# Kernel optimization log

Hardware: AMD Instinct MI355X
Metric: run time of the kernel (lower is better)

The kernel has to match this reference:

```python
import jax, jax.numpy as jnp
import numpy as np

N, E, H, R = 20000, 400000, 128, 20


def setup_inputs() -> dict:
    key = jax.random.key(0)
    ks = jax.random.split(key, 12)
    inv_h = 1.0 / np.sqrt(H)
    inv_r = 1.0 / np.sqrt(R)
    return {
        "s": jax.random.normal(ks[0], (N, H), jnp.float32),
        "v": jax.random.normal(ks[1], (N, 3, H), jnp.float32),
        "edge_rbf": jax.random.normal(ks[2], (E, R), jnp.float32),
        "edge_cutoff": jax.random.uniform(ks[3], (E,), jnp.float32),
        "edge_vec": jax.random.normal(ks[4], (E, 3), jnp.float32),
        "W1": jax.random.normal(ks[5], (H, H), jnp.float32) * inv_h,
        "b1": jnp.zeros((H,), jnp.float32),
        "W2": jax.random.normal(ks[6], (H, 3 * H), jnp.float32) * inv_h,
        "b2": jnp.zeros((3 * H,), jnp.float32),
        "Wr": jax.random.normal(ks[7], (R, 3 * H), jnp.float32) * inv_r,
        "br": jnp.zeros((3 * H,), jnp.float32),
        "edge_index": jax.random.randint(ks[8], (2, E), 0, N, jnp.int64),
    }


def reference(s, v, edge_rbf, edge_cutoff, edge_vec, W1, b1, W2, b2, Wr, br, edge_index):
    i, j = edge_index[0], edge_index[1]
    n = s.shape[0]
    # rbf projection modulated by cutoff: [E, 3H]
    W = (edge_rbf @ Wr + br) * edge_cutoff[:, None]
    # scalar MLP on gathered source features: [E, 3H]
    h = jax.nn.silu(s[j] @ W1 + b1)
    x = (h @ W2 + b2) * W
    x_ss, x_sv, x_vv = jnp.split(x, 3, axis=-1)  # each [E, H]
    ds = jax.ops.segment_sum(x_ss, i, num_segments=n)
    # dv1: outer product of edge direction with gated scalars -> [E,3,H]
    dv1 = jax.ops.segment_sum(x_sv[:, None, :] * edge_vec[:, :, None], i, num_segments=n)
    # equivariant term: project v_j onto edge direction, re-expand
    inner = jnp.sum(v[j] * edge_vec[:, :, None], axis=1)  # [E, H]
    dv2 = jax.ops.segment_sum((inner * x_vv)[:, None, :] * edge_vec[:, :, None], i, num_segments=n)
    return ds, dv1 + dv2
```

## Files before the change

### kernel.cpp

```cpp
#include <hip/hip_runtime.h>
#include <hip/hip_bf16.h>

#define HDIM 128
#define H3   384
#define RDIM 20
#define NPB  16
#define EPB  128

typedef unsigned short u16;
typedef unsigned int   u32;
typedef __attribute__((ext_vector_type(8))) short short8v;
typedef __attribute__((ext_vector_type(4))) float f32x4;

__device__ __forceinline__ u16 f2bf(float f) {
    __hip_bfloat16 h = __float2bfloat16(f);
    return *(u16*)&h;
}
__device__ __forceinline__ float bf2f(u16 u) {
    union { u32 i; float f; } x; x.i = (u32)u << 16; return x.f;
}
__device__ __forceinline__ float bflo(u32 u) {
    union { u32 i; float f; } x; x.i = u << 16; return x.f;
}
__device__ __forceinline__ float bfhi(u32 u) {
    union { u32 i; float f; } x; x.i = u & 0xffff0000u; return x.f;
}
__device__ __forceinline__ u32 pk(float lo, float hi) {
    return (u32)f2bf(lo) | ((u32)f2bf(hi) << 16);
}

__global__ __launch_bounds__(128) void node_mlp_kernel(
    const float* __restrict__ s, const float* __restrict__ W1,
    const float* __restrict__ b1, const float* __restrict__ W2,
    const float* __restrict__ b2, const float* __restrict__ v,
    u32* __restrict__ P3, int N)
{
    __shared__ float sS[NPB][HDIM];
    __shared__ float sH[NPB][HDIM];
    const int t  = threadIdx.x;
    const int n0 = blockIdx.x * NPB;

    #pragma unroll
    for (int n = 0; n < NPB; ++n) {
        int node = n0 + n;
        sS[n][t] = (node < N) ? s[(size_t)node * HDIM + t] : 0.f;
    }
    __syncthreads();

    float acc[NPB];
    #pragma unroll
    for (int n = 0; n < NPB; ++n) acc[n] = 0.f;
    for (int k = 0; k < HDIM; ++k) {
        float w = W1[k * HDIM + t];
        #pragma unroll
        for (int n = 0; n < NPB; ++n) acc[n] += sS[n][k] * w;
    }
    float bb = b1[t];
    #pragma unroll
    for (int n = 0; n < NPB; ++n) {
        float z = acc[n] + bb;
        sH[n][t] = z / (1.f + __expf(-z));
    }
    __syncthreads();

    float a0[NPB], a1[NPB], a2[NPB];
    #pragma unroll
    for (int n = 0; n < NPB; ++n) { a0[n] = 0.f; a1[n] = 0.f; a2[n] = 0.f; }
    for (int k2 = 0; k2 < HDIM / 2; ++k2) {
        float2 hv[NPB];
        #pragma unroll
        for (int n = 0; n < NPB; ++n) hv[n] = ((const float2*)sH[n])[k2];
        #pragma unroll
        for (int kk = 0; kk < 2; ++kk) {
            int k = 2 * k2 + kk;
            float w0 = W2[k * H3 + t];
            float w1 = W2[k * H3 + t + 128];
            float w2 = W2[k * H3 + t + 256];
            #pragma unroll
            for (int n = 0; n < NPB; ++n) {
                float h = kk ? hv[n].y : hv[n].x;
                a0[n] += h * w0;
                a1[n] += h * w1;
                a2[n] += h * w2;
            }
        }
    }
    float c0 = b2[t], c1 = b2[t + 128], c2 = b2[t + 256];
    #pragma unroll
    for (int n = 0; n < NPB; ++n) {
        int node = n0 + n;
        if (node < N) {
            size_t vb = (size_t)node * H3;
            float vx = v[vb + t], vy = v[vb + 128 + t], vz = v[vb + 256 + t];
            size_t pb = (size_t)node * H3 + t;
            P3[pb]       = pk(a0[n] + c0, a1[n] + c1);
            P3[pb + 128] = pk(a2[n] + c2, vx);
            P3[pb + 256] = pk(vy, vz);
        }
    }
}

__global__ void hist_kernel(const int* __restrict__ eidx, int* __restrict__ counts, int E)
{
    int e = blockIdx.x * 256 + threadIdx.x;
    if (e < E) atomicAdd(&counts[eidx[e]], 1);
}

__global__ __launch_bounds__(1024) void scan_kernel(
    const int* __restrict__ counts, int* __restrict__ rstart,
    int* __restrict__ cursor, int N)
{
    __shared__ int part[1024];
    const int t = threadIdx.x;
    const int C = 20;
    int loc[C];
    int s = 0;
    #pragma unroll
    for (int q = 0; q < C; ++q) {
        int idx = t * C + q;
        int c = (idx < N) ? counts[idx] : 0;
        loc[q] = s; s += c;
    }
    part[t] = s;
    __syncthreads();
    for (int off = 1; off < 1024; off <<= 1) {
        int vv = (t >= off) ? part[t - off] : 0;
        __syncthreads();
        part[t] += vv;
        __syncthreads();
    }
    int boff = (t > 0) ? part[t - 1] : 0;
    #pragma unroll
    for (int q = 0; q < C; ++q) {
        int idx = t * C + q;
        if (idx < N) {
            int st = boff + loc[q];
            rstart[idx] = st;
            cursor[idx] = st;
        }
    }
    if (t == 1023) rstart[N] = part[1023];
}

__global__ void scatter_kernel(const int* __restrict__ eidx, int* __restrict__ cursor,
                               int* __restrict__ eord, int E)
{
    int e = blockIdx.x * 256 + threadIdx.x;
    if (e < E) {
        int i = eidx[e];
        int pos = atomicAdd(&cursor[i], 1);
        eord[pos] = e;
    }
}

__global__ __launch_bounds__(256) void wgemm_kernel(
    const int* __restrict__ eord, const float* __restrict__ rbf,
    const float* __restrict__ cutoff, const float* __restrict__ Wr,
    const float* __restrict__ br, u16* __restrict__ Ws, int E)
{
    const int lane    = threadIdx.x & 63;
    const int wave    = threadIdx.x >> 6;
    const int g       = lane >> 4;
    const int m       = lane & 15;
    const int colhalf = wave & 1;
    const int wgrp    = wave >> 1;

    short8v bfrag[12];
    float   brt[12];
    #pragma unroll
    for (int n = 0; n < 12; ++n) {
        int col = colhalf * 192 + n * 16 + m;
        short8v f;
        #pragma unroll
        for (int j = 0; j < 8; ++j) {
            int k = 8 * g + j;
            f[j] = (k < RDIM) ? (short)f2bf(Wr[k * H3 + col]) : (short)0;
        }
        bfrag[n] = f;
        brt[n] = br[col];
    }

    const int PBI = 256;
    for (int it = 0; it < PBI / 32; ++it) {
        int pbase = blockIdx.x * PBI + it * 32 + wgrp * 16;
        if (pbase >= E) break;

        short8v af;
        int posA = pbase + m;
        if (posA < E && g < 3) {
            const float* rr = rbf + (size_t)eord[posA] * RDIM;
            if (g < 2) {
                float4 r0 = *(const float4*)(rr + 8 * g);
                float4 r1 = *(const float4*)(rr + 8 * g + 4);
                af[0] = (short)f2bf(r0.x); af[1] = (short)f2bf(r0.y);
                af[2] = (short)f2bf(r0.z); af[3] = (short)f2bf(r0.w);
                af[4] = (short)f2bf(r1.x); af[5] = (short)f2bf(r1.y);
                af[6] = (short)f2bf(r1.z); af[7] = (short)f2bf(r1.w);
            } else {
                float4 r0 = *(const float4*)(rr + 16);
                af[0] = (short)f2bf(r0.x); af[1] = (short)f2bf(r0.y);
                af[2] = (short)f2bf(r0.z); af[3] = (short)f2bf(r0.w);
                af[4] = 0; af[5] = 0; af[6] = 0; af[7] = 0;
            }
        } else {
            #pragma unroll
            for (int j = 0; j < 8; ++j) af[j] = 0;
        }

        float cut[4];
        #pragma unroll
        for (int r = 0; r < 4; ++r) {
            int pos = pbase + 4 * g + r;
            cut[r] = (pos < E) ? cutoff[eord[pos]] : 0.f;
        }

        #pragma unroll
        for (int n = 0; n < 12; ++n) {
            f32x4 c = {0.f, 0.f, 0.f, 0.f};
            c = __builtin_amdgcn_mfma_f32_16x16x32_bf16(af, bfrag[n], c, 0, 0, 0);
            int col = colhalf * 192 + n * 16 + m;
            #pragma unroll
            for (int r = 0; r < 4; ++r) {
                int pos = pbase + 4 * g + r;
                if (pos < E)
                    Ws[(size_t)pos * H3 + col] = f2bf((c[r] + brt[n]) * cut[r]);
            }
        }
    }
}

__global__ __launch_bounds__(128) void edge_kernel(
    const int* __restrict__ eord, const int* __restrict__ eidx,
    const float* __restrict__ evec, const u16* __restrict__ Ws,
    const u32* __restrict__ P3, float* __restrict__ ds,
    float* __restrict__ dv, int E)
{
    const int t    = threadIdx.x;
    const int base = blockIdx.x * EPB;
    const int cnt  = min(EPB, E - base);

    __shared__ int   sI[EPB], sJ[EPB];
    __shared__ float sVx[EPB], sVy[EPB], sVz[EPB];

    if (t < cnt) {
        int e  = eord[base + t];
        sI[t]  = eidx[e];
        sJ[t]  = eidx[E + e] * H3;
        sVx[t] = evec[3 * e];
        sVy[t] = evec[3 * e + 1];
        sVz[t] = evec[3 * e + 2];
    }
    __syncthreads();

    const u16* wp = Ws + (size_t)base * H3 + t;

    int   cur  = sI[0];
    float accs = 0.f, accx = 0.f, accy = 0.f, accz = 0.f;

    u32 ca, cb, cc; u16 w0c, w1c, w2c;
    {
        int idx = sJ[0] + t;
        ca = P3[idx]; cb = P3[idx + 128]; cc = P3[idx + 256];
        w0c = wp[0]; w1c = wp[128]; w2c = wp[256];
    }

    for (int q = 0; q < cnt; ++q) {
        u32 na = 0, nb = 0, nc = 0; u16 w0n = 0, w1n = 0, w2n = 0;
        if (q + 1 < cnt) {
            int idx = sJ[q + 1] + t;
            na = P3[idx]; nb = P3[idx + 128]; nc = P3[idx + 256];
            const u16* wq = wp + (size_t)(q + 1) * H3;
            w0n = wq[0]; w1n = wq[128]; w2n = wq[256];
        }
        if (sI[q] != cur) {
            atomicAdd(&ds[(size_t)cur * HDIM + t], accs);
            size_t dvi = (size_t)cur * H3;
            atomicAdd(&dv[dvi + t],       accx);
            atomicAdd(&dv[dvi + 128 + t], accy);
            atomicAdd(&dv[dvi + 256 + t], accz);
            accs = accx = accy = accz = 0.f;
            cur = sI[q];
        }
        float w0 = bf2f(w0c), w1 = bf2f(w1c), w2 = bf2f(w2c);
        float ex = sVx[q], ey = sVy[q], ez = sVz[q];
        float pss = bflo(ca), psv = bfhi(ca);
        float pvv = bflo(cb), vx  = bfhi(cb);
        float vy  = bflo(cc), vz  = bfhi(cc);
        float xss = w0 * pss;
        float xsv = w1 * psv;
        float xvv = w2 * pvv;
        float inner = vx * ex + vy * ey + vz * ez;
        float coef  = xsv + inner * xvv;
        accs += xss;
        accx += coef * ex;
        accy += coef * ey;
        accz += coef * ez;
        ca = na; cb = nb; cc = nc;
        w0c = w0n; w1c = w1n; w2c = w2n;
    }
    atomicAdd(&ds[(size_t)cur * HDIM + t], accs);
    size_t dvi = (size_t)cur * H3;
    atomicAdd(&dv[dvi + t],       accx);
    atomicAdd(&dv[dvi + 128 + t], accy);
    atomicAdd(&dv[dvi + 256 + t], accz);
}

__global__ __launch_bounds__(128, 4) void edge_stream_fallback(
    const int* __restrict__ eord, const int* __restrict__ eidx,
    const float* __restrict__ rbf, const float* __restrict__ cutoff,
    const float* __restrict__ evec, const float* __restrict__ Wr,
    const float* __restrict__ br, const u32* __restrict__ P3,
    float* __restrict__ ds, float* __restrict__ dv, int E)
{
    const int t    = threadIdx.x;
    const int base = blockIdx.x * 64;
    const int cnt  = min(64, E - base);

    float wr[3 * RDIM];
    #pragma unroll
    for (int k = 0; k < RDIM; ++k) {
        wr[k]            = Wr[k * H3 + t];
        wr[RDIM + k]     = Wr[k * H3 + t + 128];
        wr[2 * RDIM + k] = Wr[k * H3 + t + 256];
    }
    const float br0 = br[t], br1 = br[t + 128], br2 = br[t + 256];

    __shared__ int   sI[64], sJ[64];
    __shared__ float sCut[64], sVx[64], sVy[64], sVz[64];
    __shared__ __attribute__((aligned(16))) float sRbf[64][RDIM];

    if (t < cnt) {
        int e   = eord[base + t];
        sI[t]   = eidx[e];
        sJ[t]   = eidx[E + e] * H3;
        sCut[t] = cutoff[e];
        sVx[t]  = evec[3 * e];
        sVy[t]  = evec[3 * e + 1];
        sVz[t]  = evec[3 * e + 2];
        const float4* rr = (const float4*)(rbf + (size_t)e * RDIM);
        float4* dst = (float4*)sRbf[t];
        #pragma unroll
        for (int j = 0; j < 5; ++j) dst[j] = rr[j];
    }
    __syncthreads();

    u32 ca, cb, cc;
    {
        int idx = sJ[0] + t;
        ca = P3[idx]; cb = P3[idx + 128]; cc = P3[idx + 256];
    }
    int   cur  = sI[0];
    float accs = 0.f, accx = 0.f, accy = 0.f, accz = 0.f;

    for (int q = 0; q < cnt; ++q) {
        u32 na = 0, nb = 0, nc = 0;
        if (q + 1 < cnt) {
            int idx = sJ[q + 1] + t;
            na = P3[idx]; nb = P3[idx + 128]; nc = P3[idx + 256];
        }
        if (sI[q] != cur) {
            atomicAdd(&ds[(size_t)cur * HDIM + t], accs);
            size_t dvi = (size_t)cur * H3;
            atomicAdd(&dv[dvi + t],       accx);
            atomicAdd(&dv[dvi + 128 + t], accy);
            atomicAdd(&dv[dvi + 256 + t], accz);
            accs = accx = accy = accz = 0.f;
            cur = sI[q];
        }
        const float4* r4 = (const float4*)sRbf[q];
        float w0 = 0.f, w1 = 0.f, w2 = 0.f;
        #pragma unroll
        for (int k4 = 0; k4 < 5; ++k4) {
            float4 r = r4[k4];
            w0 += r.x*wr[4*k4]        + r.y*wr[4*k4+1]        + r.z*wr[4*k4+2]        + r.w*wr[4*k4+3];
            w1 += r.x*wr[RDIM+4*k4]   + r.y*wr[RDIM+4*k4+1]   + r.z*wr[RDIM+4*k4+2]   + r.w*wr[RDIM+4*k4+3];
            w2 += r.x*wr[2*RDIM+4*k4] + r.y*wr[2*RDIM+4*k4+1] + r.z*wr[2*RDIM+4*k4+2] + r.w*wr[2*RDIM+4*k4+3];
        }
        float cu = sCut[q];
        float ex = sVx[q], ey = sVy[q], ez = sVz[q];
        float pss = bflo(ca), psv = bfhi(ca);
        float pvv = bflo(cb), vx  = bfhi(cb);
        float vy  = bflo(cc), vz  = bfhi(cc);
        float xss = (w0 + br0) * cu * pss;
        float xsv = (w1 + br1) * cu * psv;
        float xvv = (w2 + br2) * cu * pvv;
        float inner = vx * ex + vy * ey + vz * ez;
        float coef  = xsv + inner * xvv;
        accs += xss;
        accx += coef * ex;
        accy += coef * ey;
        accz += coef * ez;
        ca = na; cb = nb; cc = nc;
    }
    atomicAdd(&ds[(size_t)cur * HDIM + t], accs);
    size_t dvi = (size_t)cur * H3;
    atomicAdd(&dv[dvi + t],       accx);
    atomicAdd(&dv[dvi + 128 + t], accy);
    atomicAdd(&dv[dvi + 256 + t], accz);
}

extern "C" void kernel_launch(void* const* d_in, const int* in_sizes, int n_in,
                              void* d_out, int out_size, void* d_ws, size_t ws_size,
                              hipStream_t stream)
{
    const float* s    = (const float*)d_in[0];
    const float* v    = (const float*)d_in[1];
    const float* rbf  = (const float*)d_in[2];
    const float* cut  = (const float*)d_in[3];
    const float* evec = (const float*)d_in[4];
    const float* W1   = (const float*)d_in[5];
    const float* b1   = (const float*)d_in[6];
    const float* W2   = (const float*)d_in[7];
    const float* b2   = (const float*)d_in[8];
    const float* Wr   = (const float*)d_in[9];
    const float* br   = (const float*)d_in[10];
    const int*   eidx = (const int*)d_in[11];

    const int N = in_sizes[0] / HDIM;
    const int E = in_sizes[3];

    float* out = (float*)d_out;
    float* ds  = out;
    float* dv  = out + (size_t)N * HDIM;

    char* w0 = (char*)d_ws;
    char* w  = w0;
    u32* P3 = (u32*)w;                     w += ((size_t)N * H3 * 4 + 255) / 256 * 256;
    int* counts = (int*)w;                 w += ((size_t)N * 4 + 255) / 256 * 256;
    int* rstart = (int*)w;                 w += ((size_t)(N + 1) * 4 + 255) / 256 * 256;
    int* cursor = (int*)w;                 w += ((size_t)N * 4 + 255) / 256 * 256;
    int* eord   = (int*)w;                 w += ((size_t)E * 4 + 255) / 256 * 256;
    u16* Ws     = (u16*)w;                 w += (size_t)E * H3 * 2;
    bool haveWs = ((size_t)(w - w0) <= ws_size);

    hipMemsetAsync(d_out, 0, (size_t)out_size * sizeof(float), stream);
    hipMemsetAsync(counts, 0, (size_t)N * sizeof(int), stream);

    node_mlp_kernel<<<(N + NPB - 1) / NPB, 128, 0, stream>>>(s, W1, b1, W2, b2, v, P3, N);
    hist_kernel<<<(E + 255) / 256, 256, 0, stream>>>(eidx, counts, E);
    scan_kernel<<<1, 1024, 0, stream>>>(counts, rstart, cursor, N);
    scatter_kernel<<<(E + 255) / 256, 256, 0, stream>>>(eidx, cursor, eord, E);

    if (haveWs) {
        wgemm_kernel<<<(E + 255) / 256, 256, 0, stream>>>(eord, rbf, cut, Wr, br, Ws, E);
        edge_kernel<<<(E + EPB - 1) / EPB, 128, 0, stream>>>(eord, eidx, evec, Ws, P3,
                                                             ds, dv, E);
    } else {
        edge_stream_fallback<<<(E + 63) / 64, 128, 0, stream>>>(eord, eidx, rbf, cut,
                                                                evec, Wr, br, P3,
                                                                ds, dv, E);
    }
}
```

Baseline: 319.8 us.

## Chunk edge-weight GEMM and edge pass so the bf16 weight buffer stays cache-resident

Splits the edge range into chunks of at most about 100K edges and runs the wgemm and edge kernels alternately per chunk. The per-edge bf16 weight buffer then occupies at most about 77MB instead of about 307MB, so it can stay in the last-level cache between the write and the read. The chunk size is derived from available workspace, so the fast path now also runs when the full buffer would not fit. The cost is more kernel launches and smaller grids per launch, which leaves less parallelism at each chunk tail.

```diff
diff --git a/kernel.cpp b/kernel.cpp
--- a/kernel.cpp
+++ b/kernel.cpp
@@ -156,7 +156,7 @@
 __global__ __launch_bounds__(256) void wgemm_kernel(
     const int* __restrict__ eord, const float* __restrict__ rbf,
     const float* __restrict__ cutoff, const float* __restrict__ Wr,
-    const float* __restrict__ br, u16* __restrict__ Ws, int E)
+    const float* __restrict__ br, u16* __restrict__ Ws, int cb, int cnt)
 {
     const int lane    = threadIdx.x & 63;
     const int wave    = threadIdx.x >> 6;
@@ -181,14 +181,15 @@
     }
 
     const int PBI = 256;
+    #pragma unroll 1
     for (int it = 0; it < PBI / 32; ++it) {
         int pbase = blockIdx.x * PBI + it * 32 + wgrp * 16;
-        if (pbase >= E) break;
+        if (pbase >= cnt) break;
 
         short8v af;
         int posA = pbase + m;
-        if (posA < E && g < 3) {
-            const float* rr = rbf + (size_t)eord[posA] * RDIM;
+        if (posA < cnt && g < 3) {
+            const float* rr = rbf + (size_t)eord[cb + posA] * RDIM;
             if (g < 2) {
                 float4 r0 = *(const float4*)(rr + 8 * g);
                 float4 r1 = *(const float4*)(rr + 8 * g + 4);
@@ -211,7 +212,7 @@
         #pragma unroll
         for (int r = 0; r < 4; ++r) {
             int pos = pbase + 4 * g + r;
-            cut[r] = (pos < E) ? cutoff[eord[pos]] : 0.f;
+            cut[r] = (pos < cnt) ? cutoff[eord[cb + pos]] : 0.f;
         }
 
         #pragma unroll
@@ -222,7 +223,7 @@
             #pragma unroll
             for (int r = 0; r < 4; ++r) {
                 int pos = pbase + 4 * g + r;
-                if (pos < E)
+                if (pos < cnt)
                     Ws[(size_t)pos * H3 + col] = f2bf((c[r] + brt[n]) * cut[r]);
             }
         }
@@ -233,17 +234,17 @@
     const int* __restrict__ eord, const int* __restrict__ eidx,
     const float* __restrict__ evec, const u16* __restrict__ Ws,
     const u32* __restrict__ P3, float* __restrict__ ds,
-    float* __restrict__ dv, int E)
-{
-    const int t    = threadIdx.x;
-    const int base = blockIdx.x * EPB;
-    const int cnt  = min(EPB, E - base);
+    float* __restrict__ dv, int cb, int ccnt, int E)
+{
+    const int t     = threadIdx.x;
+    const int lbase = blockIdx.x * EPB;
+    const int cnt   = min(EPB, ccnt - lbase);
 
     __shared__ int   sI[EPB], sJ[EPB];
     __shared__ float sVx[EPB], sVy[EPB], sVz[EPB];
 
     if (t < cnt) {
-        int e  = eord[base + t];
+        int e  = eord[cb + lbase + t];
         sI[t]  = eidx[e];
         sJ[t]  = eidx[E + e] * H3;
         sVx[t] = evec[3 * e];
@@ -252,15 +253,15 @@
     }
     __syncthreads();
 
-    const u16* wp = Ws + (size_t)base * H3 + t;
+    const u16* wp = Ws + (size_t)lbase * H3 + t;
 
     int   cur  = sI[0];
     float accs = 0.f, accx = 0.f, accy = 0.f, accz = 0.f;
 
-    u32 ca, cb, cc; u16 w0c, w1c, w2c;
+    u32 ca, cb_, cc; u16 w0c, w1c, w2c;
     {
         int idx = sJ[0] + t;
-        ca = P3[idx]; cb = P3[idx + 128]; cc = P3[idx + 256];
+        ca = P3[idx]; cb_ = P3[idx + 128]; cc = P3[idx + 256];
         w0c = wp[0]; w1c = wp[128]; w2c = wp[256];
     }
 
@@ -284,8 +285,8 @@
         float w0 = bf2f(w0c), w1 = bf2f(w1c), w2 = bf2f(w2c);
         float ex = sVx[q], ey = sVy[q], ez = sVz[q];
         float pss = bflo(ca), psv = bfhi(ca);
-        float pvv = bflo(cb), vx  = bfhi(cb);
-        float vy  = bflo(cc), vz  = bfhi(cc);
+        float pvv = bflo(cb_), vx = bfhi(cb_);
+        float vy  = bflo(cc),  vz = bfhi(cc);
         float xss = w0 * pss;
         float xsv = w1 * psv;
         float xvv = w2 * pvv;
@@ -295,7 +296,7 @@
         accx += coef * ex;
         accy += coef * ey;
         accz += coef * ez;
-        ca = na; cb = nb; cc = nc;
+        ca = na; cb_ = nb; cc = nc;
         w0c = w0n; w1c = w1n; w2c = w2n;
     }
     atomicAdd(&ds[(size_t)cur * HDIM + t], accs);
@@ -430,8 +431,14 @@
     int* rstart = (int*)w;                 w += ((size_t)(N + 1) * 4 + 255) / 256 * 256;
     int* cursor = (int*)w;                 w += ((size_t)N * 4 + 255) / 256 * 256;
     int* eord   = (int*)w;                 w += ((size_t)E * 4 + 255) / 256 * 256;
-    u16* Ws     = (u16*)w;                 w += (size_t)E * H3 * 2;
-    bool haveWs = ((size_t)(w - w0) <= ws_size);
+    u16* Ws     = (u16*)w;
+    size_t fixed = (size_t)(w - w0);
+    size_t avail = (ws_size > fixed) ? (ws_size - fixed) : 0;
+    long long Cll = (long long)(avail / (H3 * 2));
+    Cll = (Cll / EPB) * EPB;
+    if (Cll > 100352) Cll = 100352;
+    int Cchunk = (int)Cll;
+    bool haveWs = (Cchunk >= 32768);
 
     hipMemsetAsync(d_out, 0, (size_t)out_size * sizeof(float), stream);
     hipMemsetAsync(counts, 0, (size_t)N * sizeof(int), stream);
@@ -442,9 +449,13 @@
     scatter_kernel<<<(E + 255) / 256, 256, 0, stream>>>(eidx, cursor, eord, E);
 
     if (haveWs) {
-        wgemm_kernel<<<(E + 255) / 256, 256, 0, stream>>>(eord, rbf, cut, Wr, br, Ws, E);
-        edge_kernel<<<(E + EPB - 1) / EPB, 128, 0, stream>>>(eord, eidx, evec, Ws, P3,
-                                                             ds, dv, E);
+        for (int cb = 0; cb < E; cb += Cchunk) {
+            int cnt = min(Cchunk, E - cb);
+            wgemm_kernel<<<(cnt + 255) / 256, 256, 0, stream>>>(eord, rbf, cut, Wr, br,
+                                                                Ws, cb, cnt);
+            edge_kernel<<<(cnt + EPB - 1) / EPB, 128, 0, stream>>>(eord, eidx, evec, Ws,
+                                                                   P3, ds, dv, cb, cnt, E);
+        }
     } else {
         edge_stream_fallback<<<(E + 63) / 64, 128, 0, stream>>>(eord, eidx, rbf, cut,
                                                                 evec, Wr, br, P3,
```

After: 792.2 us. 2.48x slower.
